# Optimization experiments

Measured on AMD Instinct MI355X. Metric: run time of the kernel, lower is better.

## Reference

```python
import jax, jax.numpy as jnp
import numpy as np

HID = 256
NCLASS = 5
DEPTH = 11          # complete binary tree, N = 2**DEPTH - 1 nodes
BATCH = 128
N_NODES = 2 ** DEPTH - 1


def setup_inputs() -> dict:
    key = jax.random.key(0)
    ks = jax.random.split(key, 16)
    scale = 0.1
    def mat(k, shape):
        return scale * jax.random.normal(k, shape, dtype=jnp.float32)
    inp = {
        "x": jax.random.normal(ks[0], (BATCH, N_NODES, HID), dtype=jnp.float32),
        "W_i": mat(ks[1], (HID, HID)),
        "U_i": mat(ks[2], (2, HID, HID)),
        "b_i": jnp.zeros((HID,), jnp.float32),
        "W_f": mat(ks[3], (HID, HID)),
        "U_f": mat(ks[4], (2, 2, HID, HID)),
        "b_f": jnp.zeros((HID,), jnp.float32),
        "W_o": mat(ks[5], (HID, HID)),
        "U_o": mat(ks[6], (2, HID, HID)),
        "b_o": jnp.zeros((HID,), jnp.float32),
        "W_u": mat(ks[7], (HID, HID)),
        "U_u": mat(ks[8], (2, HID, HID)),
        "b_u": jnp.zeros((HID,), jnp.float32),
        "W_s": mat(ks[9], (NCLASS, HID)),
        "b_s": jnp.zeros((NCLASS,), jnp.float32),
    }
    return inp


def _mv(W, v):
    # W: [h,h] (or [c,h]), v: [B,M,h] -> [B,M,h_out]; matches U.mul(h).sum(dim=1)
    return jnp.einsum('ij,bmj->bmi', W, v)


def _tree_lstm(x, W_i, U_i, b_i, W_f, U_f, b_f, W_o, U_o, b_o, W_u, U_u, b_u):
    B, N, h = x.shape
    D = int(round(np.log2(N + 1)))
    h_all = jnp.zeros_like(x)   # init_tree: node_h = zeros
    c_all = jnp.zeros_like(x)   # init_tree: cell   = zeros
    for lvl in range(D - 1, -1, -1):  # bottom-up over tree levels
        s = 2 ** lvl - 1
        e = 2 ** (lvl + 1) - 1
        M = e - s
        x_lvl = x[:, s:e]                      # [B,M,h]
        if lvl == D - 1:  # leaves: children states are the zero-initialized ones
            hL = hR = cL = cR = jnp.zeros((B, M, h), x.dtype)
        else:
            # children of node i=s+j are at e+2j (left) and e+2j+1 (right)
            hc = h_all[:, e:e + 2 * M].reshape(B, M, 2, h)
            cc = c_all[:, e:e + 2 * M].reshape(B, M, 2, h)
            hL, hR = hc[:, :, 0], hc[:, :, 1]
            cL, cR = cc[:, :, 0], cc[:, :, 1]
        i_g = jax.nn.sigmoid(_mv(W_i, x_lvl) + _mv(U_i[0], hL) + _mv(U_i[1], hR) + b_i)
        o_g = jax.nn.sigmoid(_mv(W_o, x_lvl) + _mv(U_o[0], hL) + _mv(U_o[1], hR) + b_o)
        u_g = jnp.tanh(_mv(W_u, x_lvl) + _mv(U_u[0], hL) + _mv(U_u[1], hR) + b_u)
        Wfx = _mv(W_f, x_lvl)
        f0 = jax.nn.sigmoid(Wfx + _mv(U_f[0, 0], hL) + _mv(U_f[0, 1], hR) + b_f)
        f1 = jax.nn.sigmoid(Wfx + _mv(U_f[1, 0], hL) + _mv(U_f[1, 1], hR) + b_f)
        c_lvl = i_g * u_g + f0 * cL + f1 * cR
        h_lvl = o_g * jnp.tanh(c_lvl)
        h_all = h_all.at[:, s:e].set(h_lvl)
        c_all = c_all.at[:, s:e].set(c_lvl)
    return h_all


def reference(x, W_i, U_i, b_i, W_f, U_f, b_f, W_o, U_o, b_o, W_u, U_u, b_u, W_s, b_s):
    h_all = _tree_lstm(x, W_i, U_i, b_i, W_f, U_f, b_f, W_o, U_o, b_o, W_u, U_u, b_u)
    # PredictUpTree (dropout omitted for the deterministic reference):
    logits = jnp.einsum('ch,bnh->bnc', W_s, h_all) + b_s   # [B,N,Nclass]
    return jax.nn.softmax(logits, axis=-1)
```

## Files before the change

### kernel.cpp

```cpp
#include <hip/hip_runtime.h>
#include <math.h>

#define HID 256
#define NCLASS 5
#define DEPTH 11
#define NB 128
#define NN 2047

typedef __attribute__((ext_vector_type(8))) short bf16x8_t;
typedef __attribute__((ext_vector_type(4))) float f32x4_t;

__device__ __forceinline__ float bf2f(unsigned short u) {
    return __uint_as_float(((unsigned)u) << 16);
}
__device__ __forceinline__ unsigned short f2bf(float f) {
    unsigned x = __float_as_uint(f);
    unsigned r = (x + 0x7fff + ((x >> 16) & 1)) >> 16;
    return (unsigned short)r;
}
__device__ __forceinline__ float sigmoidf_(float x) {
    return __fdividef(1.0f, 1.0f + __expf(-x));
}
__device__ __forceinline__ float tanhf_(float x) {
    return 1.0f - __fdividef(2.0f, __expf(2.0f * x) + 1.0f);
}
__device__ __forceinline__ void gl_lds16(const void* g, void* l) {
    __builtin_amdgcn_global_load_lds(
        (const __attribute__((address_space(1))) unsigned int*)g,
        (__attribute__((address_space(3))) unsigned int*)l,
        16, 0, 0);
}

__global__ __launch_bounds__(256)
void prep_wcat(const float* __restrict__ W_i, const float* __restrict__ U_i,
               const float* __restrict__ W_f, const float* __restrict__ U_f,
               const float* __restrict__ W_o, const float* __restrict__ U_o,
               const float* __restrict__ W_u, const float* __restrict__ U_u,
               unsigned short* __restrict__ Wcat)
{
    int idx = blockIdx.x * 256 + threadIdx.x;
    int k = idx % 768;
    int n = idx / 768;
    int g = n >> 8;
    int ch = n & 255;
    int seg = k >> 8;
    int kk = k & 255;
    float v;
    if (seg == 0) {
        const float* W = (g == 0) ? W_i : (g == 1) ? W_o : (g == 2) ? W_u : W_f;
        v = W[ch * 256 + kk];
    } else {
        int side = seg - 1;
        if (g == 0)      v = U_i[(side * 256 + ch) * 256 + kk];
        else if (g == 1) v = U_o[(side * 256 + ch) * 256 + kk];
        else if (g == 2) v = U_u[(side * 256 + ch) * 256 + kk];
        else             v = U_f[(((g - 3) * 2 + side) * 256 + ch) * 256 + kk];
    }
    Wcat[(size_t)n * 768 + k] = f2bf(v);
}

__global__ __launch_bounds__(256)
void cast_x_kernel(const float* __restrict__ x, unsigned short* __restrict__ xb)
{
    size_t i = ((size_t)blockIdx.x * 256 + threadIdx.x) * 8;
    float4 a = *(const float4*)(x + i);
    float4 b = *(const float4*)(x + i + 4);
    unsigned short o[8] = {f2bf(a.x), f2bf(a.y), f2bf(a.z), f2bf(a.w),
                           f2bf(b.x), f2bf(b.y), f2bf(b.z), f2bf(b.w)};
    *(uint4*)(xb + i) = *(uint4*)o;
}

template<int NG, int NK, bool LEAF>
__global__ __launch_bounds__(512, 4)
void level_gemm(const unsigned short* __restrict__ xb,
                const unsigned short* __restrict__ hA,
                const unsigned short* __restrict__ Wcat,
                const float* __restrict__ c_child,
                const float* __restrict__ b_i, const float* __restrict__ b_o,
                const float* __restrict__ b_u, const float* __restrict__ b_f,
                float* __restrict__ c_out,
                unsigned short* __restrict__ hA_parent,
                unsigned short* __restrict__ h_all,
                int lgM)
{
    constexpr int NT = NG * 4;
    constexpr int BOFF = 8192;
    constexpr int BUFSZ = BOFF + NT * 1024;
    __shared__ __align__(16) char smem[2 * BUFSZ];

    const int tid  = threadIdx.x;
    const int w    = tid >> 6, lane = tid & 63;
    const int quad = lane >> 4, p = lane & 15;
    const int rh = w & 1, cq = w >> 1;
    const int chblk = blockIdx.x;
    const int R0 = blockIdx.y * 128;
    const int M = 1 << lgM, s = M - 1;

    const int arow = R0 + w * 16 + p;
    const int ab = arow >> lgM, am = arow & (M - 1);
    const unsigned short* a_x = xb + ((size_t)ab * NN + s + am) * 256 + quad * 8;
    const unsigned short* a_h = LEAF ? (const unsigned short*)nullptr
                                     : hA + (size_t)arow * 512 + quad * 8;
    const int nbt = LEAF ? (w < 4 ? 2 : 1) : (w < 4 ? 3 : 2);
    const int t0  = LEAF ? (w < 4 ? w * 2 : 8 + (w - 4))
                         : (w < 4 ? w * 3 : 12 + (w - 4) * 2);
    const unsigned short* bsrc[3];
    #pragma unroll
    for (int j = 0; j < 3; ++j) {
        int t = t0 + ((j < nbt) ? j : 0);
        int n = (t >> 2) * 256 + chblk * 64 + (t & 3) * 16 + p;
        bsrc[j] = Wcat + (size_t)n * 768 + quad * 8;
    }

    f32x4_t acc[4][NG];
    #pragma unroll
    for (int mi = 0; mi < 4; ++mi)
        #pragma unroll
        for (int j = 0; j < NG; ++j)
            acc[mi][j] = (f32x4_t){0.f, 0.f, 0.f, 0.f};

    {
        gl_lds16(a_x, smem + w * 1024);
        #pragma unroll
        for (int j = 0; j < 3; ++j)
            if (j < nbt) gl_lds16(bsrc[j], smem + BOFF + (t0 + j) * 1024);
    }
    __builtin_amdgcn_sched_barrier(0);

    for (int step = 0; step < NK; ++step) {
        char* bufc = smem + (size_t)(step & 1) * BUFSZ;
        if (step + 1 < NK) {
            char* bufn = smem + (size_t)((step + 1) & 1) * BUFSZ;
            const int k0 = (step + 1) * 32;
            const unsigned short* asrc = (LEAF || k0 < 256) ? (a_x + k0) : (a_h + (k0 - 256));
            gl_lds16(asrc, bufn + w * 1024);
            #pragma unroll
            for (int j = 0; j < 3; ++j)
                if (j < nbt) gl_lds16(bsrc[j] + k0, bufn + BOFF + (t0 + j) * 1024);
            __builtin_amdgcn_sched_barrier(0);
            if (nbt == 3)      asm volatile("s_waitcnt vmcnt(4)" ::: "memory");
            else if (nbt == 2) asm volatile("s_waitcnt vmcnt(3)" ::: "memory");
            else               asm volatile("s_waitcnt vmcnt(2)" ::: "memory");
        } else {
            asm volatile("s_waitcnt vmcnt(0)" ::: "memory");
        }
        __builtin_amdgcn_s_barrier();
        __builtin_amdgcn_sched_barrier(0);

        bf16x8_t af[4];
        #pragma unroll
        for (int mi = 0; mi < 4; ++mi)
            af[mi] = *(const bf16x8_t*)(bufc + ((rh * 4 + mi) * 64 + lane) * 16);
        __builtin_amdgcn_s_setprio(1);
        #pragma unroll
        for (int j = 0; j < NG; ++j) {
            bf16x8_t bfr = *(const bf16x8_t*)(bufc + BOFF + ((j * 4 + cq) * 64 + lane) * 16);
            #pragma unroll
            for (int mi = 0; mi < 4; ++mi)
                acc[mi][j] = __builtin_amdgcn_mfma_f32_16x16x32_bf16(af[mi], bfr, acc[mi][j], 0, 0, 0);
        }
        __builtin_amdgcn_s_setprio(0);
        __builtin_amdgcn_sched_barrier(0);
        __builtin_amdgcn_s_barrier();
        __builtin_amdgcn_sched_barrier(0);
    }

    const int gch = chblk * 64 + cq * 16 + p;
    const float bi = b_i[gch], bo = b_o[gch], bu = b_u[gch];
    const float bfv = LEAF ? 0.f : b_f[gch];

    #pragma unroll
    for (int mi = 0; mi < 4; ++mi) {
        const int rowq = R0 + rh * 64 + mi * 16 + quad * 4;
        #pragma unroll
        for (int reg = 0; reg < 4; ++reg) {
            const int grow = rowq + reg;
            const int b = grow >> lgM, m = grow & (M - 1);
            float ig = sigmoidf_(acc[mi][0][reg] + bi);
            float og = sigmoidf_(acc[mi][1][reg] + bo);
            float ug = tanhf_(acc[mi][2][reg] + bu);
            float c;
            if (LEAF) {
                c = ig * ug;
            } else {
                const float* crow = c_child + ((size_t)b * (M << 1) + 2 * m) * 256 + gch;
                float f0 = sigmoidf_(acc[mi][3][reg] + bfv);
                float f1 = sigmoidf_(acc[mi][4][reg] + bfv);
                c = fmaf(f0, crow[0], fmaf(f1, crow[256], ig * ug));
            }
            float h = og * tanhf_(c);
            c_out[(size_t)grow * 256 + gch] = c;
            unsigned short hb = f2bf(h);
            h_all[((size_t)b * NN + s + m) * 256 + gch] = hb;
            if (hA_parent)
                hA_parent[((size_t)b * (M >> 1) + (m >> 1)) * 512 + (m & 1) * 256 + gch] = hb;
        }
    }
}

__global__ __launch_bounds__(256)
void softmax_kernel(const unsigned short* __restrict__ h_all,
                    const float* __restrict__ W_s, const float* __restrict__ b_s,
                    float* __restrict__ out)
{
    __shared__ float Ws[5 * 256];
    int tid = threadIdx.x;
    for (int i = tid; i < 1280; i += 256) Ws[i] = W_s[i];
    __syncthreads();

    int r = tid >> 3, q = tid & 7;
    size_t row = (size_t)blockIdx.x * 32 + r;
    const unsigned short* hp = h_all + row * 256 + q * 32;

    float p0 = 0.f, p1 = 0.f, p2 = 0.f, p3 = 0.f, p4 = 0.f;
    #pragma unroll
    for (int kk = 0; kk < 32; kk += 8) {
        uint4 raw = *(const uint4*)(hp + kk);
        unsigned short hu[8];
        *(uint4*)hu = raw;
        #pragma unroll
        for (int e = 0; e < 8; ++e) {
            float hvv = bf2f(hu[e]);
            int k = q * 32 + kk + e;
            p0 = fmaf(Ws[k],        hvv, p0);
            p1 = fmaf(Ws[256 + k],  hvv, p1);
            p2 = fmaf(Ws[512 + k],  hvv, p2);
            p3 = fmaf(Ws[768 + k],  hvv, p3);
            p4 = fmaf(Ws[1024 + k], hvv, p4);
        }
    }
    #pragma unroll
    for (int off = 4; off; off >>= 1) {
        p0 += __shfl_down(p0, off, 8);
        p1 += __shfl_down(p1, off, 8);
        p2 += __shfl_down(p2, off, 8);
        p3 += __shfl_down(p3, off, 8);
        p4 += __shfl_down(p4, off, 8);
    }
    if (q == 0) {
        float l0 = p0 + b_s[0], l1 = p1 + b_s[1], l2 = p2 + b_s[2];
        float l3 = p3 + b_s[3], l4 = p4 + b_s[4];
        float mx = fmaxf(fmaxf(fmaxf(l0, l1), fmaxf(l2, l3)), l4);
        float e0 = __expf(l0 - mx), e1 = __expf(l1 - mx), e2 = __expf(l2 - mx);
        float e3 = __expf(l3 - mx), e4 = __expf(l4 - mx);
        float inv = 1.0f / (e0 + e1 + e2 + e3 + e4);
        float* orow = out + row * NCLASS;
        orow[0] = e0 * inv;
        orow[1] = e1 * inv;
        orow[2] = e2 * inv;
        orow[3] = e3 * inv;
        orow[4] = e4 * inv;
    }
}

extern "C" void kernel_launch(void* const* d_in, const int* in_sizes, int n_in,
                              void* d_out, int out_size, void* d_ws, size_t ws_size,
                              hipStream_t stream) {
    const float* x   = (const float*)d_in[0];
    const float* W_i = (const float*)d_in[1];
    const float* U_i = (const float*)d_in[2];
    const float* b_i = (const float*)d_in[3];
    const float* W_f = (const float*)d_in[4];
    const float* U_f = (const float*)d_in[5];
    const float* b_f = (const float*)d_in[6];
    const float* W_o = (const float*)d_in[7];
    const float* U_o = (const float*)d_in[8];
    const float* b_o = (const float*)d_in[9];
    const float* W_u = (const float*)d_in[10];
    const float* U_u = (const float*)d_in[11];
    const float* b_u = (const float*)d_in[12];
    const float* W_s = (const float*)d_in[13];
    const float* b_s = (const float*)d_in[14];
    float* out = (float*)d_out;

    char* p = (char*)d_ws;
    unsigned short* Wcat  = (unsigned short*)p; p += 2097152;
    unsigned short* xb    = (unsigned short*)p; p += 134152192;
    unsigned short* h_all = (unsigned short*)p; p += 134152192;
    unsigned short* hA0   = (unsigned short*)p; p += 33554432;
    unsigned short* hA1   = (unsigned short*)p; p += 67108864;
    float* cb0 = (float*)p; p += 134217728;
    float* cb1 = (float*)p; p += 67108864;

    prep_wcat<<<3840, 256, 0, stream>>>(W_i, U_i, W_f, U_f, W_o, U_o, W_u, U_u, Wcat);
    cast_x_kernel<<<32752, 256, 0, stream>>>(x, xb);

    for (int lvl = DEPTH - 1; lvl >= 0; --lvl) {
        dim3 grid(4, 1 << lvl);
        float* c_o        = (lvl & 1) ? cb1 : cb0;
        const float* c_ch = ((lvl + 1) & 1) ? cb1 : cb0;
        const unsigned short* hA_this = (lvl & 1) ? hA1 : hA0;
        unsigned short* hA_par = (lvl > 0) ? (((lvl - 1) & 1) ? hA1 : hA0) : nullptr;

        if (lvl == DEPTH - 1) {
            level_gemm<3, 8, true><<<grid, 512, 0, stream>>>(
                xb, nullptr, Wcat, nullptr, b_i, b_o, b_u, b_f,
                c_o, hA_par, h_all, lvl);
        } else {
            level_gemm<5, 24, false><<<grid, 512, 0, stream>>>(
                xb, hA_this, Wcat, c_ch, b_i, b_o, b_u, b_f,
                c_o, hA_par, h_all, lvl);
        }
    }

    softmax_kernel<<<8188, 256, 0, stream>>>(h_all, W_s, b_s, out);
}
```

Before: 1.262 ms.

## Read children directly from h_all/c_all, swizzle blocks, add small-level GEMM kernel

Drops the separate packed parent-h buffers and ping-pong c buffers. Each level now reads left and right child h and c straight from full-size h_all/c_all arrays, so the extra hA_parent scatter store per element goes away. Blocks are remapped to a 1D grid with a swizzle that groups 8 row-blocks per channel block, to improve L2 reuse of weights and activations. The top levels (lvl<4) use a new small_gemm kernel with one wave per 16x16 tile and register double-buffering instead of the 512-thread LDS kernel, to raise parallelism when there are few rows. The trade-off is a larger c_all footprint and less contiguous child reads.

```diff
diff --git a/kernel.cpp b/kernel.cpp
--- a/kernel.cpp
+++ b/kernel.cpp
@@ -73,15 +73,12 @@
 template<int NG, int NK, bool LEAF>
 __global__ __launch_bounds__(512, 4)
 void level_gemm(const unsigned short* __restrict__ xb,
-                const unsigned short* __restrict__ hA,
                 const unsigned short* __restrict__ Wcat,
-                const float* __restrict__ c_child,
+                float* __restrict__ c_all,
+                unsigned short* __restrict__ h_all,
                 const float* __restrict__ b_i, const float* __restrict__ b_o,
                 const float* __restrict__ b_u, const float* __restrict__ b_f,
-                float* __restrict__ c_out,
-                unsigned short* __restrict__ hA_parent,
-                unsigned short* __restrict__ h_all,
-                int lgM)
+                int lgM, int nrb)
 {
     constexpr int NT = NG * 4;
     constexpr int BOFF = 8192;
@@ -92,15 +89,28 @@
     const int w    = tid >> 6, lane = tid & 63;
     const int quad = lane >> 4, p = lane & 15;
     const int rh = w & 1, cq = w >> 1;
-    const int chblk = blockIdx.x;
-    const int R0 = blockIdx.y * 128;
-    const int M = 1 << lgM, s = M - 1;
+
+    int chblk, rb;
+    {
+        int bid = blockIdx.x;
+        if ((nrb & 7) == 0) {
+            int x = bid & 7, sl = bid >> 3;
+            chblk = sl & 3;
+            rb = x + 8 * (sl >> 2);
+        } else {
+            chblk = bid & 3;
+            rb = bid >> 2;
+        }
+    }
+    const int R0 = rb * 128;
+    const int M = 1 << lgM, s = M - 1, s2 = 2 * M - 1;
 
     const int arow = R0 + w * 16 + p;
     const int ab = arow >> lgM, am = arow & (M - 1);
     const unsigned short* a_x = xb + ((size_t)ab * NN + s + am) * 256 + quad * 8;
-    const unsigned short* a_h = LEAF ? (const unsigned short*)nullptr
-                                     : hA + (size_t)arow * 512 + quad * 8;
+    const unsigned short* a_hL = LEAF ? a_x
+        : h_all + ((size_t)ab * NN + s2 + 2 * am) * 256 + quad * 8;
+    const unsigned short* a_hR = a_hL + 256;
     const int nbt = LEAF ? (w < 4 ? 2 : 1) : (w < 4 ? 3 : 2);
     const int t0  = LEAF ? (w < 4 ? w * 2 : 8 + (w - 4))
                          : (w < 4 ? w * 3 : 12 + (w - 4) * 2);
@@ -112,6 +122,16 @@
         bsrc[j] = Wcat + (size_t)n * 768 + quad * 8;
     }
 
+    auto stage_step = [&](int k0, char* buf) {
+        const unsigned short* asrc =
+            (LEAF || k0 < 256) ? (a_x + k0)
+            : (k0 < 512 ? (a_hL + (k0 - 256)) : (a_hR + (k0 - 512)));
+        gl_lds16(asrc, buf + w * 1024);
+        #pragma unroll
+        for (int j = 0; j < 3; ++j)
+            if (j < nbt) gl_lds16(bsrc[j] + k0, buf + BOFF + (t0 + j) * 1024);
+    };
+
     f32x4_t acc[4][NG];
     #pragma unroll
     for (int mi = 0; mi < 4; ++mi)
@@ -119,24 +139,14 @@
         for (int j = 0; j < NG; ++j)
             acc[mi][j] = (f32x4_t){0.f, 0.f, 0.f, 0.f};
 
-    {
-        gl_lds16(a_x, smem + w * 1024);
-        #pragma unroll
-        for (int j = 0; j < 3; ++j)
-            if (j < nbt) gl_lds16(bsrc[j], smem + BOFF + (t0 + j) * 1024);
-    }
+    stage_step(0, smem);
     __builtin_amdgcn_sched_barrier(0);
 
     for (int step = 0; step < NK; ++step) {
         char* bufc = smem + (size_t)(step & 1) * BUFSZ;
         if (step + 1 < NK) {
             char* bufn = smem + (size_t)((step + 1) & 1) * BUFSZ;
-            const int k0 = (step + 1) * 32;
-            const unsigned short* asrc = (LEAF || k0 < 256) ? (a_x + k0) : (a_h + (k0 - 256));
-            gl_lds16(asrc, bufn + w * 1024);
-            #pragma unroll
-            for (int j = 0; j < 3; ++j)
-                if (j < nbt) gl_lds16(bsrc[j] + k0, bufn + BOFF + (t0 + j) * 1024);
+            stage_step((step + 1) * 32, bufn);
             __builtin_amdgcn_sched_barrier(0);
             if (nbt == 3)      asm volatile("s_waitcnt vmcnt(4)" ::: "memory");
             else if (nbt == 2) asm volatile("s_waitcnt vmcnt(3)" ::: "memory");
@@ -172,6 +182,17 @@
     #pragma unroll
     for (int mi = 0; mi < 4; ++mi) {
         const int rowq = R0 + rh * 64 + mi * 16 + quad * 4;
+        float cl[4], cr[4];
+        if (!LEAF) {
+            #pragma unroll
+            for (int reg = 0; reg < 4; ++reg) {
+                const int grow = rowq + reg;
+                const int b = grow >> lgM, m = grow & (M - 1);
+                const float* crow = c_all + ((size_t)b * NN + s2 + 2 * m) * 256 + gch;
+                cl[reg] = crow[0];
+                cr[reg] = crow[256];
+            }
+        }
         #pragma unroll
         for (int reg = 0; reg < 4; ++reg) {
             const int grow = rowq + reg;
@@ -183,18 +204,94 @@
             if (LEAF) {
                 c = ig * ug;
             } else {
-                const float* crow = c_child + ((size_t)b * (M << 1) + 2 * m) * 256 + gch;
                 float f0 = sigmoidf_(acc[mi][3][reg] + bfv);
                 float f1 = sigmoidf_(acc[mi][4][reg] + bfv);
-                c = fmaf(f0, crow[0], fmaf(f1, crow[256], ig * ug));
+                c = fmaf(f0, cl[reg], fmaf(f1, cr[reg], ig * ug));
             }
             float h = og * tanhf_(c);
-            c_out[(size_t)grow * 256 + gch] = c;
-            unsigned short hb = f2bf(h);
-            h_all[((size_t)b * NN + s + m) * 256 + gch] = hb;
-            if (hA_parent)
-                hA_parent[((size_t)b * (M >> 1) + (m >> 1)) * 512 + (m & 1) * 256 + gch] = hb;
-        }
+            c_all[((size_t)b * NN + s + m) * 256 + gch] = c;
+            h_all[((size_t)b * NN + s + m) * 256 + gch] = f2bf(h);
+        }
+    }
+}
+
+__global__ __launch_bounds__(256)
+void small_gemm(const unsigned short* __restrict__ xb,
+                const unsigned short* __restrict__ Wcat,
+                float* __restrict__ c_all,
+                unsigned short* __restrict__ h_all,
+                const float* __restrict__ b_i, const float* __restrict__ b_o,
+                const float* __restrict__ b_u, const float* __restrict__ b_f,
+                int lgM)
+{
+    const int tid = threadIdx.x, w = tid >> 6, lane = tid & 63;
+    const int quad = lane >> 4, p = lane & 15;
+    const int wid = blockIdx.x * 4 + w;
+    const int mt = wid >> 4, ct = wid & 15;
+    const int r0 = mt * 16, ch0 = ct * 16;
+    const int M = 1 << lgM, s = M - 1, s2 = 2 * M - 1;
+
+    const int arow = r0 + p, ab = arow >> lgM, am = arow & (M - 1);
+    const unsigned short* axp = xb + ((size_t)ab * NN + s + am) * 256 + quad * 8;
+    const unsigned short* ahL = h_all + ((size_t)ab * NN + s2 + 2 * am) * 256 + quad * 8;
+    const unsigned short* ahR = ahL + 256;
+    const unsigned short* bbp[5];
+    #pragma unroll
+    for (int j = 0; j < 5; ++j)
+        bbp[j] = Wcat + (size_t)(j * 256 + ch0 + p) * 768 + quad * 8;
+
+    f32x4_t acc[5];
+    #pragma unroll
+    for (int j = 0; j < 5; ++j) acc[j] = (f32x4_t){0.f, 0.f, 0.f, 0.f};
+
+    bf16x8_t fa0, fa1, fb0[5], fb1[5];
+
+    #define SLOAD(k0, fa, fb)                                                    \
+        fa = *(const bf16x8_t*)((k0) < 256 ? (axp + (k0))                        \
+                 : (k0) < 512 ? (ahL + ((k0) - 256)) : (ahR + ((k0) - 512)));    \
+        _Pragma("unroll")                                                        \
+        for (int j = 0; j < 5; ++j) fb[j] = *(const bf16x8_t*)(bbp[j] + (k0));
+    #define SCOMP(fa, fb)                                                        \
+        _Pragma("unroll")                                                        \
+        for (int j = 0; j < 5; ++j)                                              \
+            acc[j] = __builtin_amdgcn_mfma_f32_16x16x32_bf16(fa, fb[j], acc[j], 0, 0, 0);
+
+    SLOAD(0, fa0, fb0);
+    SLOAD(32, fa1, fb1);
+    #pragma unroll
+    for (int st = 0; st < 24; st += 2) {
+        SCOMP(fa0, fb0);
+        if (st + 2 < 24) { SLOAD((st + 2) * 32, fa0, fb0); }
+        SCOMP(fa1, fb1);
+        if (st + 3 < 24) { SLOAD((st + 3) * 32, fa1, fb1); }
+    }
+    #undef SLOAD
+    #undef SCOMP
+
+    const int gch = ch0 + p;
+    const float bi = b_i[gch], bo = b_o[gch], bu = b_u[gch], bfv = b_f[gch];
+    float cl[4], cr[4];
+    #pragma unroll
+    for (int reg = 0; reg < 4; ++reg) {
+        const int grow = r0 + quad * 4 + reg;
+        const int b = grow >> lgM, m = grow & (M - 1);
+        const float* crow = c_all + ((size_t)b * NN + s2 + 2 * m) * 256 + gch;
+        cl[reg] = crow[0];
+        cr[reg] = crow[256];
+    }
+    #pragma unroll
+    for (int reg = 0; reg < 4; ++reg) {
+        const int grow = r0 + quad * 4 + reg;
+        const int b = grow >> lgM, m = grow & (M - 1);
+        float ig = sigmoidf_(acc[0][reg] + bi);
+        float og = sigmoidf_(acc[1][reg] + bo);
+        float ug = tanhf_(acc[2][reg] + bu);
+        float f0 = sigmoidf_(acc[3][reg] + bfv);
+        float f1 = sigmoidf_(acc[4][reg] + bfv);
+        float c = fmaf(f0, cl[reg], fmaf(f1, cr[reg], ig * ug));
+        float h = og * tanhf_(c);
+        c_all[((size_t)b * NN + s + m) * 256 + gch] = c;
+        h_all[((size_t)b * NN + s + m) * 256 + gch] = f2bf(h);
     }
 }
 
@@ -277,29 +374,22 @@
     unsigned short* Wcat  = (unsigned short*)p; p += 2097152;
     unsigned short* xb    = (unsigned short*)p; p += 134152192;
     unsigned short* h_all = (unsigned short*)p; p += 134152192;
-    unsigned short* hA0   = (unsigned short*)p; p += 33554432;
-    unsigned short* hA1   = (unsigned short*)p; p += 67108864;
-    float* cb0 = (float*)p; p += 134217728;
-    float* cb1 = (float*)p; p += 67108864;
+    float*          c_all = (float*)p;          p += 268304384;
 
     prep_wcat<<<3840, 256, 0, stream>>>(W_i, U_i, W_f, U_f, W_o, U_o, W_u, U_u, Wcat);
     cast_x_kernel<<<32752, 256, 0, stream>>>(x, xb);
 
     for (int lvl = DEPTH - 1; lvl >= 0; --lvl) {
-        dim3 grid(4, 1 << lvl);
-        float* c_o        = (lvl & 1) ? cb1 : cb0;
-        const float* c_ch = ((lvl + 1) & 1) ? cb1 : cb0;
-        const unsigned short* hA_this = (lvl & 1) ? hA1 : hA0;
-        unsigned short* hA_par = (lvl > 0) ? (((lvl - 1) & 1) ? hA1 : hA0) : nullptr;
-
+        const int nrb = 1 << lvl;
         if (lvl == DEPTH - 1) {
-            level_gemm<3, 8, true><<<grid, 512, 0, stream>>>(
-                xb, nullptr, Wcat, nullptr, b_i, b_o, b_u, b_f,
-                c_o, hA_par, h_all, lvl);
+            level_gemm<3, 8, true><<<dim3(4 * nrb), 512, 0, stream>>>(
+                xb, Wcat, c_all, h_all, b_i, b_o, b_u, b_f, lvl, nrb);
+        } else if (lvl >= 4) {
+            level_gemm<5, 24, false><<<dim3(4 * nrb), 512, 0, stream>>>(
+                xb, Wcat, c_all, h_all, b_i, b_o, b_u, b_f, lvl, nrb);
         } else {
-            level_gemm<5, 24, false><<<grid, 512, 0, stream>>>(
-                xb, hA_this, Wcat, c_ch, b_i, b_o, b_u, b_f,
-                c_o, hA_par, h_all, lvl);
+            small_gemm<<<dim3(32 << lvl), 256, 0, stream>>>(
+                xb, Wcat, c_all, h_all, b_i, b_o, b_u, b_f, lvl);
         }
     }
 
```

Measured after the change: 1.139 ms. -9.8%, faster.
